# Kernel tuning notes

Hardware: AMD Instinct MI355X
Metric: run time of the kernel (lower is better)

## Reference

```python
import jax, jax.numpy as jnp
import numpy as np

B, R, S, P = 32768, 16, 128, 128  # particles, rotations, num_sphs, num_projections


def setup_inputs() -> dict:
    key = jax.random.key(0)
    k1, k2, k3 = jax.random.split(key, 3)
    weight_scale = np.sqrt(6.0 / (S + P))  # RandomUniform(-scale, scale) init
    x_real = jax.random.normal(k1, (B, R, S), dtype=jnp.float32)
    x_imag = jax.random.normal(k2, (B, R, S), dtype=jnp.float32)
    projection = jax.random.uniform(k3, (R, S, P), dtype=jnp.float32,
                                    minval=-weight_scale, maxval=weight_scale)
    return {"x_real": x_real, "x_imag": x_imag, "projection": projection}


def reference(x_real, x_imag, projection):
    # complex input (B, R, S); real weight (R, S, P) cast to complex64
    x = jax.lax.complex(x_real, x_imag)
    w = projection.astype(x.dtype)
    # contraction over num_sphs (fused GEMM instead of expand_dims*mul+sum)
    sph_projected = jnp.einsum('brs,rsp->brp', x, w)  # (B, R, P) complex64
    # conversion == 'abs'
    return jnp.abs(sph_projected)
```

## Files before the change

kernel.cpp:

```cpp
#include <hip/hip_runtime.h>
#include <hip/hip_bf16.h>
#include <math.h>


typedef __attribute__((ext_vector_type(8))) __bf16 bf16x8;
typedef __attribute__((ext_vector_type(4))) float f32x4;

#define R_TOT 16
#define S_TOT 128
#define P_TOT 128
#define RS 2048
#define RP 2048
#define ROWS_PER_BLOCK 256
#define STRIP 16
#define NSTRIPS 16

typedef const __attribute__((address_space(1))) void* gas_t;
typedef __attribute__((address_space(3))) void* las_t;

__global__ __launch_bounds__(256, 3) void cproj_kernel(
    const float* __restrict__ x_real,
    const float* __restrict__ x_imag,
    const float* __restrict__ proj,
    float* __restrict__ out)
{
    __shared__ __attribute__((aligned(16))) float xb[3][2][STRIP][128];

    const int tid  = threadIdx.x;
    const int bid  = blockIdx.x;
    const int r    = (bid >> 3) & 15;
    const int br   = (bid & 7) | ((bid >> 7) << 3);
    const int lane = tid & 63;
    const int wid  = tid >> 6;
    const int m    = lane & 15;
    const int g    = lane >> 4;
    const int b_base = br * ROWS_PER_BLOCK;

    const int st_arr = wid >> 1;
    const int st_r0  = (wid & 1) * 8;
    const float* xsrc = (st_arr == 0) ? x_real : x_imag;

#define STAGE(strip_)                                                         \
    do {                                                                      \
        _Pragma("unroll")                                                     \
        for (int i = 0; i < 4; ++i) {                                         \
            const int row = st_r0 + 2 * i + (lane >> 5);                      \
            const int gb  = b_base + (strip_) * STRIP + row;                  \
            const float* gp = xsrc + (size_t)gb * RS + r * S_TOT              \
                              + (((lane & 31) ^ (row & 7)) << 2);             \
            __builtin_amdgcn_global_load_lds(                                 \
                (gas_t)gp,                                                    \
                (las_t)&xb[(strip_) % 3][st_arr][st_r0 + 2 * i][0],           \
                16, 0, 0);                                                    \
        }                                                                     \
    } while (0)

    bf16x8 wf[2][4];
    {
        const float* wrp = proj + (size_t)r * (S_TOT * P_TOT) + wid * 32 + m;
        #pragma unroll
        for (int nt = 0; nt < 2; ++nt) {
            #pragma unroll
            for (int kk = 0; kk < 4; ++kk) {
                bf16x8 w;
                #pragma unroll
                for (int j = 0; j < 8; ++j) {
                    w[j] = (__bf16)wrp[(size_t)(kk * 32 + g * 8 + j) * P_TOT
                                       + nt * 16];
                }
                wf[nt][kk] = w;
            }
        }
    }
    asm volatile("s_waitcnt vmcnt(0)" ::: "memory");

    STAGE(0);
    STAGE(1);

#define ITER(s_, vm_)                                                         \
    {                                                                         \
        asm volatile("s_waitcnt vmcnt(" #vm_ ")" ::: "memory");               \
        __builtin_amdgcn_s_barrier();                                         \
        __builtin_amdgcn_sched_barrier(0);                                    \
        if ((s_) + 2 < NSTRIPS) STAGE((s_) + 2);                              \
        bf16x8 ar[2][4];                                                      \
        _Pragma("unroll")                                                     \
        for (int a = 0; a < 2; ++a) {                                         \
            _Pragma("unroll")                                                 \
            for (int kk = 0; kk < 4; ++kk) {                                  \
                const int c0  = kk * 8 + 2 * g;                               \
                const int s0i = ((c0) ^ (m & 7)) << 2;                        \
                const int s1i = ((c0 + 1) ^ (m & 7)) << 2;                    \
                f32x4 lo = *(const f32x4*)&xb[(s_) % 3][a][m][s0i];           \
                f32x4 hi = *(const f32x4*)&xb[(s_) % 3][a][m][s1i];           \
                bf16x8 t;                                                     \
                _Pragma("unroll")                                             \
                for (int j = 0; j < 4; ++j) {                                 \
                    t[j]     = (__bf16)lo[j];                                 \
                    t[j + 4] = (__bf16)hi[j];                                 \
                }                                                             \
                ar[a][kk] = t;                                                \
            }                                                                 \
        }                                                                     \
        f32x4 acc[2][2];                                     \
        acc[0][0] = (f32x4)0.0f; acc[0][1] = (f32x4)0.0f;                     \
        acc[1][0] = (f32x4)0.0f; acc[1][1] = (f32x4)0.0f;                     \
        _Pragma("unroll")                                                     \
        for (int kk = 0; kk < 4; ++kk) {                                      \
            _Pragma("unroll")                                                 \
            for (int nt = 0; nt < 2; ++nt) {                                  \
                acc[nt][0] = __builtin_amdgcn_mfma_f32_16x16x32_bf16(         \
                    ar[0][kk], wf[nt][kk], acc[nt][0], 0, 0, 0);              \
                acc[nt][1] = __builtin_amdgcn_mfma_f32_16x16x32_bf16(         \
                    ar[1][kk], wf[nt][kk], acc[nt][1], 0, 0, 0);              \
            }                                                                 \
        }                                                                     \
        float* po = out + (size_t)(b_base + (s_) * STRIP + g * 4) * RP        \
                    + r * P_TOT + wid * 32 + m;                               \
        _Pragma("unroll")                                                     \
        for (int nt = 0; nt < 2; ++nt) {                                      \
            _Pragma("unroll")                                                 \
            for (int j = 0; j < 4; ++j) {                                     \
                float re = acc[nt][0][j];                                     \
                float im = acc[nt][1][j];                                     \
                po[(size_t)j * RP + nt * 16] = sqrtf(re * re + im * im);      \
            }                                                                 \
        }                                                                     \
    }

    ITER(0, 4)
    ITER(1, 12)
    ITER(2, 20)
    ITER(3, 20)
    ITER(4, 20)
    ITER(5, 20)
    ITER(6, 20)
    ITER(7, 20)
    ITER(8, 20)
    ITER(9, 20)
    ITER(10, 20)
    ITER(11, 20)
    ITER(12, 20)
    ITER(13, 20)
    ITER(14, 20)
    ITER(15, 16)
#undef ITER
#undef STAGE
}

extern "C" void kernel_launch(void* const* d_in, const int* in_sizes, int n_in,
                              void* d_out, int out_size, void* d_ws, size_t ws_size,
                              hipStream_t stream) {
    const float* x_real = (const float*)d_in[0];
    const float* x_imag = (const float*)d_in[1];
    const float* proj   = (const float*)d_in[2];
    float* out = (float*)d_out;

    dim3 grid(R_TOT * 128);
    dim3 block(256);
    cproj_kernel<<<grid, block, 0, stream>>>(x_real, x_imag, proj, out);
}
```

Baseline: 159.0 us.

## Widen blocks to four rotations per block with double-buffered contiguous row staging

```diff
diff --git a/kernel.cpp b/kernel.cpp
--- a/kernel.cpp
+++ b/kernel.cpp
@@ -6,67 +6,68 @@
 typedef __attribute__((ext_vector_type(8))) __bf16 bf16x8;
 typedef __attribute__((ext_vector_type(4))) float f32x4;
 
-#define R_TOT 16
-#define S_TOT 128
-#define P_TOT 128
 #define RS 2048
 #define RP 2048
-#define ROWS_PER_BLOCK 256
 #define STRIP 16
 #define NSTRIPS 16
 
 typedef const __attribute__((address_space(1))) void* gas_t;
 typedef __attribute__((address_space(3))) void* las_t;
 
-__global__ __launch_bounds__(256, 3) void cproj_kernel(
+__global__ __launch_bounds__(512, 2) void cproj_kernel(
     const float* __restrict__ x_real,
     const float* __restrict__ x_imag,
     const float* __restrict__ proj,
     float* __restrict__ out)
 {
-    __shared__ __attribute__((aligned(16))) float xb[3][2][STRIP][128];
+    __shared__ __attribute__((aligned(16))) float xb[2][2][STRIP][512];
 
     const int tid  = threadIdx.x;
     const int bid  = blockIdx.x;
-    const int r    = (bid >> 3) & 15;
-    const int br   = (bid & 7) | ((bid >> 7) << 3);
+    const int r0   = (bid & 3) * 4;
+    const int b_base = (bid >> 2) * 256;
+
     const int lane = tid & 63;
     const int wid  = tid >> 6;
+    const int rr   = wid >> 1;
+    const int ph   = wid & 1;
+    const int p0   = ph * 64;
     const int m    = lane & 15;
     const int g    = lane >> 4;
-    const int b_base = br * ROWS_PER_BLOCK;
 
-    const int st_arr = wid >> 1;
-    const int st_r0  = (wid & 1) * 8;
-    const float* xsrc = (st_arr == 0) ? x_real : x_imag;
+    const int st_arr  = wid >> 2;
+    const int st_row0 = (wid & 3) * 4;
+    const float* xsrc = st_arr ? x_imag : x_real;
 
-#define STAGE(strip_)                                                         \
+#define STAGE(buf_, strip_)                                                   \
     do {                                                                      \
         _Pragma("unroll")                                                     \
-        for (int i = 0; i < 4; ++i) {                                         \
-            const int row = st_r0 + 2 * i + (lane >> 5);                      \
-            const int gb  = b_base + (strip_) * STRIP + row;                  \
-            const float* gp = xsrc + (size_t)gb * RS + r * S_TOT              \
-                              + (((lane & 31) ^ (row & 7)) << 2);             \
+        for (int i = 0; i < 8; ++i) {                                         \
+            const int row  = st_row0 + (i >> 1);                              \
+            const int half = i & 1;                                           \
+            const float* gp = xsrc                                            \
+                + (size_t)(b_base + (strip_) * STRIP + row) * RS + r0 * 128   \
+                + (((half * 64 + lane) ^ (row & 7)) << 2);                    \
             __builtin_amdgcn_global_load_lds(                                 \
-                (gas_t)gp,                                                    \
-                (las_t)&xb[(strip_) % 3][st_arr][st_r0 + 2 * i][0],           \
+                (gas_t)gp, (las_t)&xb[buf_][st_arr][row][half * 256],         \
                 16, 0, 0);                                                    \
         }                                                                     \
     } while (0)
 
-    bf16x8 wf[2][4];
+    STAGE(0, 0);
+
+    bf16x8 wf[4][4];
     {
-        const float* wrp = proj + (size_t)r * (S_TOT * P_TOT) + wid * 32 + m;
+        const float* wp = proj + (size_t)(r0 + rr) * (128 * 128) + p0 + m;
         #pragma unroll
-        for (int nt = 0; nt < 2; ++nt) {
+        for (int nt = 0; nt < 4; ++nt) {
             #pragma unroll
             for (int kk = 0; kk < 4; ++kk) {
                 bf16x8 w;
                 #pragma unroll
                 for (int j = 0; j < 8; ++j) {
-                    w[j] = (__bf16)wrp[(size_t)(kk * 32 + g * 8 + j) * P_TOT
-                                       + nt * 16];
+                    w[j] = (__bf16)wp[(size_t)(kk * 32 + g * 8 + j) * 128
+                                      + nt * 16];
                 }
                 wf[nt][kk] = w;
             }
@@ -74,25 +75,23 @@
     }
     asm volatile("s_waitcnt vmcnt(0)" ::: "memory");
 
-    STAGE(0);
-    STAGE(1);
-
-#define ITER(s_, vm_)                                                         \
+#define ITER(s_)                                                              \
     {                                                                         \
-        asm volatile("s_waitcnt vmcnt(" #vm_ ")" ::: "memory");               \
+               \
+        asm volatile("s_waitcnt vmcnt(16)" ::: "memory");                     \
         __builtin_amdgcn_s_barrier();                                         \
         __builtin_amdgcn_sched_barrier(0);                                    \
-        if ((s_) + 2 < NSTRIPS) STAGE((s_) + 2);                              \
+        if ((s_) + 1 < NSTRIPS) STAGE(((s_) + 1) & 1, (s_) + 1);              \
         bf16x8 ar[2][4];                                                      \
         _Pragma("unroll")                                                     \
         for (int a = 0; a < 2; ++a) {                                         \
             _Pragma("unroll")                                                 \
             for (int kk = 0; kk < 4; ++kk) {                                  \
-                const int c0  = kk * 8 + 2 * g;                               \
-                const int s0i = ((c0) ^ (m & 7)) << 2;                        \
-                const int s1i = ((c0 + 1) ^ (m & 7)) << 2;                    \
-                f32x4 lo = *(const f32x4*)&xb[(s_) % 3][a][m][s0i];           \
-                f32x4 hi = *(const f32x4*)&xb[(s_) % 3][a][m][s1i];           \
+                const int base = rr * 32 + kk * 8;                            \
+                const int clo  = base + ((2 * g) ^ (m & 7));                  \
+                const int chi  = base + ((2 * g + 1) ^ (m & 7));              \
+                f32x4 lo = *(const f32x4*)&xb[(s_) & 1][a][m][clo * 4];       \
+                f32x4 hi = *(const f32x4*)&xb[(s_) & 1][a][m][chi * 4];       \
                 bf16x8 t;                                                     \
                 _Pragma("unroll")                                             \
                 for (int j = 0; j < 4; ++j) {                                 \
@@ -102,23 +101,27 @@
                 ar[a][kk] = t;                                                \
             }                                                                 \
         }                                                                     \
-        f32x4 acc[2][2];                                     \
-        acc[0][0] = (f32x4)0.0f; acc[0][1] = (f32x4)0.0f;                     \
-        acc[1][0] = (f32x4)0.0f; acc[1][1] = (f32x4)0.0f;                     \
+        f32x4 acc[4][2];                                                      \
+        _Pragma("unroll")                                                     \
+        for (int nt = 0; nt < 4; ++nt) {                                      \
+            acc[nt][0] = (f32x4)0.0f;                                         \
+            acc[nt][1] = (f32x4)0.0f;                                         \
+        }                                                                     \
         _Pragma("unroll")                                                     \
         for (int kk = 0; kk < 4; ++kk) {                                      \
             _Pragma("unroll")                                                 \
-            for (int nt = 0; nt < 2; ++nt) {                                  \
+            for (int nt = 0; nt < 4; ++nt) {                                  \
                 acc[nt][0] = __builtin_amdgcn_mfma_f32_16x16x32_bf16(         \
                     ar[0][kk], wf[nt][kk], acc[nt][0], 0, 0, 0);              \
                 acc[nt][1] = __builtin_amdgcn_mfma_f32_16x16x32_bf16(         \
                     ar[1][kk], wf[nt][kk], acc[nt][1], 0, 0, 0);              \
             }                                                                 \
         }                                                                     \
+                   \
         float* po = out + (size_t)(b_base + (s_) * STRIP + g * 4) * RP        \
-                    + r * P_TOT + wid * 32 + m;                               \
+                    + (r0 + rr) * 128 + p0 + m;                               \
         _Pragma("unroll")                                                     \
-        for (int nt = 0; nt < 2; ++nt) {                                      \
+        for (int nt = 0; nt < 4; ++nt) {                                      \
             _Pragma("unroll")                                                 \
             for (int j = 0; j < 4; ++j) {                                     \
                 float re = acc[nt][0][j];                                     \
@@ -128,22 +131,22 @@
         }                                                                     \
     }
 
-    ITER(0, 4)
-    ITER(1, 12)
-    ITER(2, 20)
-    ITER(3, 20)
-    ITER(4, 20)
-    ITER(5, 20)
-    ITER(6, 20)
-    ITER(7, 20)
-    ITER(8, 20)
-    ITER(9, 20)
-    ITER(10, 20)
-    ITER(11, 20)
-    ITER(12, 20)
-    ITER(13, 20)
-    ITER(14, 20)
-    ITER(15, 16)
+    ITER(0)
+    ITER(1)
+    ITER(2)
+    ITER(3)
+    ITER(4)
+    ITER(5)
+    ITER(6)
+    ITER(7)
+    ITER(8)
+    ITER(9)
+    ITER(10)
+    ITER(11)
+    ITER(12)
+    ITER(13)
+    ITER(14)
+    ITER(15)
 #undef ITER
 #undef STAGE
 }
@@ -156,7 +159,7 @@
     const float* proj   = (const float*)d_in[2];
     float* out = (float*)d_out;
 
-    dim3 grid(R_TOT * 128);
-    dim3 block(256);
+    dim3 grid(512);
+    dim3 block(512);
     cproj_kernel<<<grid, block, 0, stream>>>(x_real, x_imag, proj, out);
 }
```

Measured after the change: 155.0 us. 1.03x faster.
